# Kernel tuning notes

Hardware: AMD Instinct MI355X
Metric: run time of the kernel (lower is better)

Reference implementation:

```python
import jax, jax.numpy as jnp
import numpy as np
from jax import lax

EPS_BN = 1e-5
EPS_LN = 1e-5
K = 16  # patch size (cubic)
S = 8   # patch stride (cubic)


def _conv3d(x, w, stride):
    # x: [B,C,D,H,W], w: [O,I,kD,kH,kW], padding=1 on all spatial dims (torch padding=1)
    return lax.conv_general_dilated(
        x, w, (stride, stride, stride), [(1, 1), (1, 1), (1, 1)],
        dimension_numbers=('NCDHW', 'OIDHW', 'NCDHW'))


def _bn_relu(x, g, b):
    # train-mode BatchNorm3d: batch statistics over (B, D, H, W) per channel
    mean = jnp.mean(x, axis=(0, 2, 3, 4), keepdims=True)
    var = jnp.var(x, axis=(0, 2, 3, 4), keepdims=True)
    xh = (x - mean) * lax.rsqrt(var + EPS_BN)
    g = g[None, :, None, None, None]
    b = b[None, :, None, None, None]
    return jax.nn.relu(xh * g + b)


def _extract_patches_3d(f0):
    # f0: [B,C,D,H,W] -> patches [B,N,C*K^3] (C-major then kD,kH,kW, matching torch unfold),
    # coords [B,N,3]
    B, C, D, H, W = f0.shape
    Do, Ho, Wo = (D - K) // S + 1, (H - K) // S + 1, (W - K) // S + 1
    di = jnp.arange(Do)[:, None] * S + jnp.arange(K)[None, :]  # [Do,K]
    hi = jnp.arange(Ho)[:, None] * S + jnp.arange(K)[None, :]
    wi = jnp.arange(Wo)[:, None] * S + jnp.arange(K)[None, :]
    p = f0[:, :, di]                 # [B,C,Do,K,H,W]
    p = p[:, :, :, :, hi]            # [B,C,Do,K,Ho,K,W]
    p = p[:, :, :, :, :, :, wi]      # [B,C,Do,K,Ho,K,Wo,K]
    p = p.transpose(0, 2, 4, 6, 1, 3, 5, 7)  # [B,Do,Ho,Wo,C,K,K,K]
    patches = p.reshape(B, Do * Ho * Wo, C * K * K * K)
    half = (K - 1) / 2.0
    z = (jnp.arange(Do) * S + half) / max(D - 1, 1)
    y = (jnp.arange(Ho) * S + half) / max(H - 1, 1)
    xg = (jnp.arange(Wo) * S + half) / max(W - 1, 1)
    zz, yy, xx = jnp.meshgrid(z, y, xg, indexing='ij')
    coords = jnp.stack([zz.reshape(-1), yy.reshape(-1), xx.reshape(-1)], axis=-1)
    coords = jnp.broadcast_to(coords[None], (B,) + coords.shape)
    return patches, coords


def _layer_norm(x, g, b):
    mu = jnp.mean(x, axis=-1, keepdims=True)
    var = jnp.var(x, axis=-1, keepdims=True)
    return (x - mu) * lax.rsqrt(var + EPS_LN) * g + b


def setup_inputs() -> dict:
    key = jax.random.key(0)
    ks = jax.random.split(key, 8)
    C_in, mid, stem, tok_d, aux_d = 1, 16, 32, 128, 32
    pdim = stem * K * K * K  # 131072
    f32 = jnp.float32
    x = jax.random.normal(ks[0], (2, C_in, 128, 128, 128), dtype=f32)
    def kinit(k, shape, fan_in):
        return jax.random.normal(k, shape, dtype=f32) * (1.0 / np.sqrt(fan_in))
    return {
        'x': x,
        'conv1_w': kinit(ks[1], (mid, C_in, 3, 3, 3), C_in * 27),
        'bn1_g': jnp.ones((mid,), f32), 'bn1_b': jnp.zeros((mid,), f32),
        'conv2_w': kinit(ks[2], (mid, mid, 3, 3, 3), mid * 27),
        'bn2_g': jnp.ones((mid,), f32), 'bn2_b': jnp.zeros((mid,), f32),
        'conv3_w': kinit(ks[3], (stem, mid, 3, 3, 3), mid * 27),
        'bn3_g': jnp.ones((stem,), f32), 'bn3_b': jnp.zeros((stem,), f32),
        'tok_w': kinit(ks[4], (tok_d, pdim), pdim), 'tok_b': jnp.zeros((tok_d,), f32),
        'aux_w': kinit(ks[5], (aux_d, pdim), pdim), 'aux_b': jnp.zeros((aux_d,), f32),
        'ln_g': jnp.ones((tok_d,), f32), 'ln_b': jnp.zeros((tok_d,), f32),
    }


def reference(x, conv1_w, bn1_g, bn1_b, conv2_w, bn2_g, bn2_b, conv3_w, bn3_g, bn3_b,
              tok_w, tok_b, aux_w, aux_b, ln_g, ln_b):
    f0 = _bn_relu(_conv3d(x, conv1_w, 1), bn1_g, bn1_b)
    f0 = _bn_relu(_conv3d(f0, conv2_w, 1), bn2_g, bn2_b)
    f0 = _bn_relu(_conv3d(f0, conv3_w, 2), bn3_g, bn3_b)  # [B,32,64,64,64]
    patches, coords = _extract_patches_3d(f0)  # [B,N,131072]
    tokens = jnp.einsum('bnp,tp->bnt', patches, tok_w) + tok_b
    tokens = _layer_norm(tokens, ln_g, ln_b)
    aux = jnp.einsum('bnp,ap->bna', patches, aux_w) + aux_b
    return tokens, aux, coords
```

## Files before the change

kernel.cpp:

```cpp
#include <hip/hip_runtime.h>
#include <hip/hip_bf16.h>


typedef __hip_bfloat16 bf16;
typedef __attribute__((ext_vector_type(8))) short short8;
typedef __attribute__((ext_vector_type(4))) float f32x4;
__device__ __forceinline__ float b2f(bf16 v){ return __bfloat162float(v); }
__device__ __forceinline__ bf16 f2b(float v){ return __float2bfloat16(v); }
__device__ __forceinline__ unsigned short f2bu(float f){
  unsigned u = __float_as_uint(f);
  return (unsigned short)((u + 0x7fff + ((u>>16)&1)) >> 16);
}
__device__ __forceinline__ unsigned cvtpk(float lo, float hi){
  unsigned r;
  asm("v_cvt_pk_bf16_f32 %0, %1, %2" : "=v"(r) : "v"(lo), "v"(hi));
  return r;
}

#define SP12 2097152
#define SP3  262144
#define M_TOT 686
#define TOK_OFF 0
#define AUX_OFF 87808
#define CRD_OFF 109760
#define KSPLIT 64
#define NSLAB 32

__global__ __launch_bounds__(256) void k_packw(const float* __restrict__ w1,
                                               const float* __restrict__ w2,
                                               const float* __restrict__ w3,
                                               unsigned short* __restrict__ wp1,
                                               unsigned short* __restrict__ wp2,
                                               unsigned short* __restrict__ wp3){
  int i = blockIdx.x*256 + threadIdx.x;
  if(i < 512){
    int oc = i>>5, k = i&31;
    float v = (k<27)? w1[oc*27+k] : 0.f;
    wp1[i] = f2bu(v);
  } else if(i < 7680){
    int j = i - 512;
    int oc = j/448, k = j - oc*448;
    int tap = k>>4, ic = k&15;
    float v = (tap<27)? w2[(oc*16+ic)*27+tap] : 0.f;
    wp2[oc*448+k] = f2bu(v);
  } else if(i < 22016){
    int j = i - 7680;
    int oc = j/448, r = j - oc*448;
    int h = r/224, k2 = r - h*224;
    int tap = (k2>>5)*4 + ((k2>>3)&3);
    int ic = h*8 + (k2&7);
    float v = (tap<27)? w3[(oc*16+ic)*27+tap] : 0.f;
    wp3[oc*448 + h*224 + k2] = f2bu(v);
  }
}

#define C1P 88
__global__ __launch_bounds__(256) void k_conv1(const float* __restrict__ x,
                                               const unsigned short* __restrict__ wp1,
                                               unsigned short* __restrict__ y1u,
                                               float* __restrict__ psum){
  __shared__ unsigned short in_l[6*6*C1P];
  int t = threadIdx.x;
  int bx = blockIdx.x;
  int xt = bx&1, yt = (bx>>1)&31, zt = (bx>>6)&31, b = bx>>11;
  int x0 = xt*64, y0 = yt*4, z0 = zt*4;

  for(int i=t; i<648; i+=256){
    int c = i%18; int row = i/18; int yy = row%6; int zz = row/6;
    int gz = z0-1+zz, gy = y0-1+yy;
    bool rowok = ((unsigned)gz<128u) && ((unsigned)gy<128u);
    int gx4 = x0-4+c*4;
    const float* rp = x + (size_t)b*SP12 + (rowok? ((gz<<14)+(gy<<7)) : 0);
    float v0,v1,v2,v3;
    if(rowok && gx4>=0 && gx4<=124){
      float4 v = *(const float4*)(rp + gx4);
      v0=v.x; v1=v.y; v2=v.z; v3=v.w;
    } else {
      float vv[4];
#pragma unroll
      for(int e=0;e<4;e++){
        int gx = gx4+e; bool ok = rowok && ((unsigned)gx<128u);
        float val = rp[ok? gx : 0];
        vv[e] = ok? val : 0.f;
      }
      v0=vv[0]; v1=vv[1]; v2=vv[2]; v3=vv[3];
    }
    uint2 p;
    p.x = cvtpk(v0,v1);
    p.y = cvtpk(v2,v3);
    *(uint2*)&in_l[row*C1P + c*4] = p;
  }
  __syncthreads();

  int lane = t&63, wv = t>>6;
  int m = lane&15, q = lane>>4;
  short8 wfr = *(const short8*)(wp1 + m*32 + q*8);
  int toff[8];
#pragma unroll
  for(int j=0;j<8;j++){
    int tap = q*8+j; if(tap>26) tap=26;
    int dz = tap/9; int rr = tap-dz*9; int dy = rr/3; int dx = rr-dy*3;
    toff[j] = (dz*6+dy)*C1P + dx + 3 + m;
  }
  float s4[4]={0.f,0.f,0.f,0.f}, q4[4]={0.f,0.f,0.f,0.f};
#pragma unroll
  for(int yi=0; yi<4; yi++){
#pragma unroll
    for(int mg=0; mg<4; mg++){
      int base = (wv*6+yi)*C1P + mg*16;
      short8 vf;
#pragma unroll
      for(int j=0;j<8;j++) vf[j] = (short)in_l[base + toff[j]];
      f32x4 acc = (f32x4){0.f,0.f,0.f,0.f};
      acc = __builtin_amdgcn_mfma_f32_16x16x32_bf16(wfr, vf, acc, 0,0,0);
      int gz = z0+wv, gy = y0+yi, gxv = x0 + mg*16 + m;
      size_t vbase = (size_t)((b<<21)|(gz<<14)|(gy<<7)|gxv);
      uint2 pw; pw.x = cvtpk(acc[0],acc[1]); pw.y = cvtpk(acc[2],acc[3]);
      *(uint2*)(y1u + vbase*16 + q*4) = pw;
#pragma unroll
      for(int reg=0; reg<4; reg++){
        float v = acc[reg];
        s4[reg] += v; q4[reg] += v*v;
      }
    }
  }
#pragma unroll
  for(int off=1; off<16; off<<=1){
#pragma unroll
    for(int rg=0;rg<4;rg++){ s4[rg] += __shfl_xor(s4[rg],off); q4[rg] += __shfl_xor(q4[rg],off); }
  }
  __syncthreads();
  float* red = (float*)in_l;
  if(m==0){
#pragma unroll
    for(int rg=0;rg<4;rg++){ red[wv*32 + q*4+rg] = s4[rg]; red[wv*32+16 + q*4+rg] = q4[rg]; }
  }
  __syncthreads();
  if(t<32){
    float tot = red[t]+red[32+t]+red[64+t]+red[96+t];
    atomicAdd(&psum[(blockIdx.x & (NSLAB-1))*64 + t], tot);
  }
}

__global__ void k_finalize(const float* __restrict__ psum, const float* __restrict__ g,
                           const float* __restrict__ bb, float* __restrict__ scsh,
                           int C, float invN){
  int i = threadIdx.x;
  if(i<C){
    float s=0.f, q=0.f;
    for(int sl=0; sl<NSLAB; sl++){ s += psum[sl*64+i]; q += psum[sl*64+C+i]; }
    float mean = s*invN;
    float var  = q*invN - mean*mean;
    float sc = g[i]*rsqrtf(var+1e-5f);
    scsh[i]   = sc;
    scsh[C+i] = bb[i] - mean*sc;
  }
}

__global__ __launch_bounds__(256) void k_conv2(const unsigned short* __restrict__ y1u,
                                               const unsigned short* __restrict__ wp2,
                                               const float* __restrict__ scsh,
                                               unsigned short* __restrict__ y2u,
                                               float* __restrict__ psum2){
  __shared__ unsigned short tile[10*6*18*16];
  __shared__ float s_sc[16], s_sh[16];
  int t = threadIdx.x;
  if(t < 32){ float v = scsh[t]; if(t<16) s_sc[t]=v; else s_sh[t-16]=v; }
  int bx = blockIdx.x;
  int txx = bx&7, tyy=(bx>>3)&31, tzz=(bx>>8)&15, b=bx>>12;
  int x0 = txx*16, y0 = tyy*4, z0 = tzz*8;

  {
    int sxl = t%18, szz = t/18;
    bool sact = t < 180;
    int gx = x0 + sxl - 1, gz = z0 + szz - 1;
    bool szok = sact && ((unsigned)gx<128u) && ((unsigned)gz<128u);
    size_t srow0 = szok ? (size_t)((b<<21)|(gz<<14)|gx) : 0;
    int sw8 = ((sxl>>2)&1)*8;
    int tb = (szz*6*18 + sxl)*16;
    __syncthreads();
    if(sact){
#pragma unroll
      for(int yy=0; yy<6; yy++){
        int gy = y0 + yy - 1;
        bool ok = szok && ((unsigned)gy < 128u);
        uint4 o0; o0.x=0;o0.y=0;o0.z=0;o0.w=0;
        uint4 o1 = o0;
        if(ok){
          const unsigned short* src = y1u + ((srow0 | ((size_t)gy<<7))<<4);
          uint4 u0 = *(const uint4*)src;
          uint4 u1 = *(const uint4*)(src+8);
          unsigned uu[8]; uu[0]=u0.x; uu[1]=u0.y; uu[2]=u0.z; uu[3]=u0.w;
          uu[4]=u1.x; uu[5]=u1.y; uu[6]=u1.z; uu[7]=u1.w;
          unsigned oo[8];
#pragma unroll
          for(int j=0;j<8;j++){
            float lo = fmaxf(__uint_as_float(uu[j]<<16)        *s_sc[2*j]   + s_sh[2*j],   0.f);
            float hi = fmaxf(__uint_as_float(uu[j]&0xffff0000u)*s_sc[2*j+1] + s_sh[2*j+1], 0.f);
            oo[j] = cvtpk(lo, hi);
          }
          o0.x=oo[0]; o0.y=oo[1]; o0.z=oo[2]; o0.w=oo[3];
          o1.x=oo[4]; o1.y=oo[5]; o1.z=oo[6]; o1.w=oo[7];
        }
        unsigned short* dst = &tile[tb + yy*288];
        *(uint4*)(dst + sw8)       = o0;
        *(uint4*)(dst + (8 - sw8)) = o1;
      }
    }
  }
  __syncthreads();

  int lane = t & 63, wid = t>>6;
  int m = lane & 15, q = lane>>4;
  int qh = q&1, qt = q>>1;
  f32x4 acc[8];
#pragma unroll
  for(int r=0;r<8;r++) acc[r] = (f32x4){0.f,0.f,0.f,0.f};
  const char* tbase = (const char*)tile + wid*6912;
  const unsigned short* wrow = wp2 + m*448 + q*8;
#pragma unroll
  for(int kp=0;kp<14;kp++){
    short8 wf = *(const short8*)(wrow + kp*32);
    int tap = kp*2 + qt; if(tap>26) tap=26;
    int dz = tap/9; int rr2 = tap - dz*9; int dy = rr2/3; int dx = rr2 - dy*3;
    int xl = m + dx;
    int abyte = ((dz*6 + dy)*18 + xl)*32 + ((qh ^ ((xl>>2)&1))*16);
    const char* ap = tbase + abyte;
#pragma unroll
    for(int r=0;r<8;r++){
      const short8 vf = *(const short8*)(ap + ((r>>2)*6 + (r&3))*576);
      acc[r] = __builtin_amdgcn_mfma_f32_16x16x32_bf16(wf, vf, acc[r], 0,0,0);
    }
  }

  float s4[4]={0.f,0.f,0.f,0.f}, q4[4]={0.f,0.f,0.f,0.f};
#pragma unroll
  for(int r=0;r<8;r++){
    int gz = z0 + wid*2 + (r>>2), gy = y0 + (r&3);
    size_t vbase = (size_t)((b<<21)|(gz<<14)|(gy<<7)|(x0+m));
    uint2 pw; pw.x = cvtpk(acc[r][0],acc[r][1]); pw.y = cvtpk(acc[r][2],acc[r][3]);
    *(uint2*)(y2u + vbase*16 + q*4) = pw;
#pragma unroll
    for(int reg=0;reg<4;reg++){
      float v = acc[r][reg];
      s4[reg] += v; q4[reg] += v*v;
    }
  }
#pragma unroll
  for(int off=1; off<16; off<<=1){
#pragma unroll
    for(int rg=0;rg<4;rg++){ s4[rg] += __shfl_xor(s4[rg],off); q4[rg] += __shfl_xor(q4[rg],off); }
  }
  __syncthreads();
  float* red = (float*)tile;
  if(m==0){
#pragma unroll
    for(int rg=0;rg<4;rg++){ red[wid*32 + q*4+rg] = s4[rg]; red[wid*32+16 + q*4+rg] = q4[rg]; }
  }
  __syncthreads();
  if(t<32){
    float tot = red[t]+red[32+t]+red[64+t]+red[96+t];
    atomicAdd(&psum2[(blockIdx.x & (NSLAB-1))*64 + t], tot);
  }
}

#define C3PITCH 576
__global__ __launch_bounds__(256) void k_conv3(const unsigned short* __restrict__ y2u,
                                               const unsigned short* __restrict__ wp3,
                                               const float* __restrict__ scsh,
                                               bf16* __restrict__ f0,
                                               float* __restrict__ psum3){
  __shared__ unsigned short tile3[45*288];
  __shared__ float s_sc[16], s_sh[16];
  int t = threadIdx.x;
  if(t < 32){ float v = scsh[t]; if(t<16) s_sc[t]=v; else s_sh[t-16]=v; }
  __syncthreads();
  int bx = blockIdx.x;
  int tx = bx&3, ty=(bx>>2)&15, tz=(bx>>6)&31, b=bx>>11;
  int x0 = tx*16, y0 = ty*4, z0 = tz*2;
  int gx0 = 2*x0-1, gy0 = 2*y0-1, gz0 = 2*z0-1;

  int lane = t & 63, wid = t>>6;
  int m = lane & 15, q = lane>>4;
  f32x4 acc[2][2];
#pragma unroll
  for(int r=0;r<2;r++){ acc[r][0]=(f32x4){0,0,0,0}; acc[r][1]=(f32x4){0,0,0,0}; }
  const unsigned short* wr0 = wp3 + m*448      + q*8;
  const unsigned short* wr1 = wp3 + (16+m)*448 + q*8;

  for(int half=0; half<2; half++){
    for(int i=t;i<1485;i+=256){
      int xl_ = i%33; int r1 = i/33; int yy_ = r1%9; int zz_ = r1/9;
      int gx = gx0+xl_, gy = gy0+yy_, gz = gz0+zz_;
      bool ok = (gx>=0)&&(gy>=0)&&(gz>=0);
      uint4 o; o.x=0;o.y=0;o.z=0;o.w=0;
      if(ok){
        uint4 u = *(const uint4*)(y2u + ((size_t)((b<<21)|(gz<<14)|(gy<<7)|gx))*16 + half*8);
        int c0 = half*8;
        unsigned uu[4]; uu[0]=u.x; uu[1]=u.y; uu[2]=u.z; uu[3]=u.w;
        unsigned oo[4];
#pragma unroll
        for(int j=0;j<4;j++){
          float lo = fmaxf(__uint_as_float(uu[j]<<16)        *s_sc[c0+2*j]   + s_sh[c0+2*j],   0.f);
          float hi = fmaxf(__uint_as_float(uu[j]&0xffff0000u)*s_sc[c0+2*j+1] + s_sh[c0+2*j+1], 0.f);
          oo[j] = cvtpk(lo, hi);
        }
        o.x=oo[0]; o.y=oo[1]; o.z=oo[2]; o.w=oo[3];
      }
      int sb = (xl_<<4) ^ ((xl_&8)<<1) ^ ((xl_&16)<<1);
      *(uint4*)((char*)tile3 + (zz_*9+yy_)*C3PITCH + sb) = o;
    }
    __syncthreads();

    const unsigned short* w0h = wr0 + half*224;
    const unsigned short* w1h = wr1 + half*224;
#pragma unroll
    for(int kp=0;kp<7;kp++){
      short8 bf0 = *(const short8*)(w0h + kp*32);
      short8 bf1 = *(const short8*)(w1h + kp*32);
      int tap = kp*4 + q; if(tap>26) tap=26;
      int dz = tap/9; int rr = tap - dz*9; int dy = rr/3; int dx = rr - dy*3;
      int xl = 2*m + dx;
      int sb = (xl<<4) ^ ((xl&8)<<1) ^ ((xl&16)<<1);
#pragma unroll
      for(int rl=0;rl<2;rl++){
        int row = wid*2 + rl;
        int tz_ = 2*(row>>2) + dz;
        int ty_ = 2*(row&3) + dy;
        const short8 af = *(const short8*)((const char*)tile3 + (tz_*9+ty_)*C3PITCH + sb);
        acc[rl][0] = __builtin_amdgcn_mfma_f32_16x16x32_bf16(af, bf0, acc[rl][0], 0,0,0);
        acc[rl][1] = __builtin_amdgcn_mfma_f32_16x16x32_bf16(af, bf1, acc[rl][1], 0,0,0);
      }
    }
    __syncthreads();
  }

  float s0=0.f,q0=0.f,s1=0.f,q1=0.f;
#pragma unroll
  for(int rl=0;rl<2;rl++){
    int row = wid*2 + rl;
    int oz = z0 + (row>>2), oy = y0 + (row&3);
    size_t sp = (size_t)oz*4096 + oy*64 + x0 + q*4;
#pragma unroll
    for(int oct=0;oct<2;oct++){
      int oc = oct*16 + m;
      bf16* dst = f0 + (size_t)(b*32+oc)*SP3 + sp;
      f32x4 a = acc[rl][oct];
      uint2 pw; pw.x = cvtpk(a[0],a[1]); pw.y = cvtpk(a[2],a[3]);
      *(uint2*)dst = pw;
#pragma unroll
      for(int reg=0;reg<4;reg++){
        float v = a[reg];
        if(oct==0){ s0 += v; q0 += v*v; } else { s1 += v; q1 += v*v; }
      }
    }
  }
  s0 += __shfl_xor(s0,16); s0 += __shfl_xor(s0,32);
  q0 += __shfl_xor(q0,16); q0 += __shfl_xor(q0,32);
  s1 += __shfl_xor(s1,16); s1 += __shfl_xor(s1,32);
  q1 += __shfl_xor(q1,16); q1 += __shfl_xor(q1,32);
  __syncthreads();
  float* red = (float*)tile3;
  if(lane<16){
    red[wid*64+lane]    = s0; red[wid*64+16+lane] = s1;
    red[wid*64+32+lane] = q0; red[wid*64+48+lane] = q1;
  }
  __syncthreads();
  if(t<64){
    float tot = red[t]+red[64+t]+red[128+t]+red[192+t];
    atomicAdd(&psum3[(blockIdx.x & (NSLAB-1))*64 + t], tot);
  }
}

__global__ __launch_bounds__(256) void k_cvtw(const float* __restrict__ tokw,
                                              const float* __restrict__ auxw,
                                              unsigned short* __restrict__ wb){
  int i = blockIdx.x*256 + threadIdx.x;
  int n = i >> 15;
  int g = i & 32767;
  const float* src = (n<128)? tokw + (size_t)n*131072 : auxw + (size_t)(n-128)*131072;
  float4 v = *(const float4*)(src + g*4);
  uint2 pw; pw.x = cvtpk(v.x, v.y); pw.y = cvtpk(v.z, v.w);
  *(uint2*)(wb + (size_t)n*131072 + g*4) = pw;
}

__global__ __launch_bounds__(256) void k_gemm(const bf16* __restrict__ f0,
                                              const unsigned short* __restrict__ wb,
                                              const float* __restrict__ scsh3,
                                              float* __restrict__ out_acc){
  __shared__ unsigned short Al[64*72];
  __shared__ unsigned short Wl[160*72];
  int mblk = blockIdx.x % 11; int ks = blockIdx.x / 11;
  int M0 = mblk*64;
  int c  = ks >> 1; int kh = ks & 1;
  float sc = scsh3[c], sh = scsh3[32+c];
  int t = threadIdx.x;
  int lane = t & 63; int wid = t >> 6;
  int wm = (wid & 1)*32; int wn = (wid >> 1)*80;
  f32x4 acc[2][5];
#pragma unroll
  for(int i=0;i<2;i++)
#pragma unroll
    for(int j=0;j<5;j++) acc[i][j] = (f32x4){0.f,0.f,0.f,0.f};

  int ky_off0 = (t&7)>>1, half0 = t&1;
  int m_a = t>>3;
  int mg1 = M0 + m_a;       if(mg1>685) mg1=685;
  int mg2 = M0 + m_a + 32;  if(mg2>685) mg2=685;
  int b1 = mg1/343, r1 = mg1%343;
  int b2 = mg2/343, r2 = mg2%343;
  int sp1 = ((r1/49)*8)*4096 + (((r1/7)%7)*8)*64 + (r1%7)*8;
  int sp2 = ((r2/49)*8)*4096 + (((r2/7)%7)*8)*64 + (r2%7)*8;
  const bf16* f0c1 = f0 + (size_t)(b1*32+c)*SP3;
  const bf16* f0c2 = f0 + (size_t)(b2*32+c)*SP3;

  for(int bk=0; bk<32; bk++){
    int bk2 = kh*32 + bk;
    int kz = bk2>>2; int kyb = (bk2&3)*4;
    __syncthreads();
#pragma unroll
    for(int p=0;p<5;p++){
      int n = p*32 + (t>>3);
      int koff = (t&7)*8;
      uint4 v = *(const uint4*)(wb + (size_t)n*131072 + c*4096 + bk2*64 + koff);
      *(uint4*)&Wl[n*72 + koff] = v;
    }
    {
      int ky = kyb + ky_off0; int xo = half0*8;
      int ldso = ky_off0*16 + half0*8;
      uint4 u1 = *(const uint4*)(f0c1 + sp1 + kz*4096 + ky*64 + xo);
      uint4 u2 = *(const uint4*)(f0c2 + sp2 + kz*4096 + ky*64 + xo);
      unsigned uu[8]; uu[0]=u1.x; uu[1]=u1.y; uu[2]=u1.z; uu[3]=u1.w;
      uu[4]=u2.x; uu[5]=u2.y; uu[6]=u2.z; uu[7]=u2.w;
      unsigned outw[8];
#pragma unroll
      for(int qq=0;qq<8;qq++){
        float lo = fmaxf(__uint_as_float(uu[qq]<<16)*sc + sh, 0.f);
        float hi = fmaxf(__uint_as_float(uu[qq]&0xffff0000u)*sc + sh, 0.f);
        outw[qq] = cvtpk(lo, hi);
      }
      uint4 w1; w1.x=outw[0]; w1.y=outw[1]; w1.z=outw[2]; w1.w=outw[3];
      uint4 w2; w2.x=outw[4]; w2.y=outw[5]; w2.z=outw[6]; w2.w=outw[7];
      *(uint4*)&Al[m_a*72 + ldso] = w1;
      *(uint4*)&Al[(m_a+32)*72 + ldso] = w2;
    }
    __syncthreads();
#pragma unroll
    for(int kstep=0;kstep<2;kstep++){
      int ko = kstep*32 + (lane>>4)*8;
      short8 af[2], bfr[5];
#pragma unroll
      for(int mt=0;mt<2;mt++)
        af[mt] = *(const short8*)&Al[(wm + mt*16 + (lane&15))*72 + ko];
#pragma unroll
      for(int nt=0;nt<5;nt++)
        bfr[nt] = *(const short8*)&Wl[(wn + nt*16 + (lane&15))*72 + ko];
#pragma unroll
      for(int mt=0;mt<2;mt++)
#pragma unroll
        for(int nt=0;nt<5;nt++)
          acc[mt][nt] = __builtin_amdgcn_mfma_f32_16x16x32_bf16(af[mt], bfr[nt], acc[mt][nt], 0,0,0);
    }
  }
#pragma unroll
  for(int mt=0;mt<2;mt++){
    int mb = M0 + wm + mt*16 + (lane>>4)*4;
#pragma unroll
    for(int nt=0;nt<5;nt++){
      int n = wn + nt*16 + (lane&15);
#pragma unroll
      for(int reg=0;reg<4;reg++){
        int mm = mb + reg;
        if(mm < M_TOT)
          out_acc[((size_t)ks*M_TOT + mm)*160 + n] = acc[mt][nt][reg];
      }
    }
  }
}

__global__ __launch_bounds__(256) void k_final(const float* __restrict__ out_acc,
                                               const float* __restrict__ tok_b,
                                               const float* __restrict__ aux_b,
                                               const float* __restrict__ ln_g,
                                               const float* __restrict__ ln_b,
                                               float* __restrict__ out){
  int m = blockIdx.x;
  int n = threadIdx.x;
  __shared__ float sA[128], sB[128];
  float sum = 0.f;
  if(n < 160){
    for(int ks=0;ks<KSPLIT;ks++) sum += out_acc[((size_t)ks*M_TOT+m)*160 + n];
  }
  float tval = 0.f;
  if(n < 128){
    tval = sum + tok_b[n];
    sA[n] = tval; sB[n] = tval*tval;
  }
  __syncthreads();
  for(int s=64;s>0;s>>=1){
    if(n < s){ sA[n] += sA[n+s]; sB[n] += sB[n+s]; }
    __syncthreads();
  }
  float mean = sA[0]*(1.f/128.f);
  float var  = sB[0]*(1.f/128.f) - mean*mean;
  float rstd = rsqrtf(var + 1e-5f);
  if(n<128){
    out[TOK_OFF + (size_t)m*128 + n] = (tval-mean)*rstd*ln_g[n] + ln_b[n];
  } else if(n<160){
    out[AUX_OFF + (size_t)m*32 + (n-128)] = sum + aux_b[n-128];
  } else if(n<163){
    int j = n-160;
    int pn = m % 343;
    int nz = pn/49, ny=(pn/7)%7, nx=pn%7;
    int g = (j==0)? nz : (j==1)? ny : nx;
    out[CRD_OFF + (size_t)m*3 + j] = (g*8 + 7.5f)*(1.f/63.f);
  }
}

extern "C" void kernel_launch(void* const* d_in, const int* in_sizes, int n_in,
                              void* d_out, int out_size, void* d_ws, size_t ws_size,
                              hipStream_t stream){
  const float* x    = (const float*)d_in[0];
  const float* w1   = (const float*)d_in[1];
  const float* g1   = (const float*)d_in[2];
  const float* b1   = (const float*)d_in[3];
  const float* w2   = (const float*)d_in[4];
  const float* g2   = (const float*)d_in[5];
  const float* b2   = (const float*)d_in[6];
  const float* w3   = (const float*)d_in[7];
  const float* g3   = (const float*)d_in[8];
  const float* b3   = (const float*)d_in[9];
  const float* tokw = (const float*)d_in[10];
  const float* tokb = (const float*)d_in[11];
  const float* auxw = (const float*)d_in[12];
  const float* auxb = (const float*)d_in[13];
  const float* lng  = (const float*)d_in[14];
  const float* lnb  = (const float*)d_in[15];
  float* out = (float*)d_out;

  char* ws = (char*)d_ws;
  unsigned short* y1u = (unsigned short*)ws;
  unsigned short* y2u = (unsigned short*)(ws + 134217728);
  bf16*  f0      = (bf16*)ws;
  float* out_acc = (float*)(ws + 33554432);
  unsigned short* wbf = (unsigned short*)(ws + 67108864);
  float* stats   = (float*)d_out;
  float* psum1 = stats;        float* psum2 = stats+2048; float* psum3 = stats+4096;
  float* scsh1 = stats+6144;   float* scsh2 = stats+6208; float* scsh3 = stats+6272;
  unsigned short* wp2 = (unsigned short*)(stats + 8192);
  unsigned short* wp3 = (unsigned short*)(stats + 12288);
  unsigned short* wp1 = (unsigned short*)(stats + 20480);

  hipMemsetAsync(stats, 0, 6144*sizeof(float), stream);

  k_packw<<<86, 256, 0, stream>>>(w1, w2, w3, wp1, wp2, wp3);
  k_conv1<<<4096, 256, 0, stream>>>(x, wp1, y1u, psum1);
  k_finalize<<<1, 64, 0, stream>>>(psum1, g1, b1, scsh1, 16, 1.f/4194304.f);
  k_conv2<<<8192, 256, 0, stream>>>(y1u, wp2, scsh1, y2u, psum2);
  k_finalize<<<1, 64, 0, stream>>>(psum2, g2, b2, scsh2, 16, 1.f/4194304.f);
  k_conv3<<<4096, 256, 0, stream>>>(y2u, wp3, scsh2, f0, psum3);
  k_finalize<<<1, 64, 0, stream>>>(psum3, g3, b3, scsh3, 32, 1.f/524288.f);
  k_cvtw<<<20480, 256, 0, stream>>>(tokw, auxw, wbf);
  k_gemm<<<704, 256, 0, stream>>>(f0, wbf, scsh3, out_acc);
  k_final<<<686, 256, 0, stream>>>(out_acc, tokb, auxb, lng, lnb, out);
}
```

Baseline: 458.4 us.

## Fuse fp32-to-bf16 weight conversion into GEMM load and remap blocks per XCD

Removes the separate weight conversion kernel and its bf16 weight buffer; the GEMM now loads fp32 token/aux weights and converts them to bf16 while filling shared memory. Blocks are also remapped so that the blocks sharing a K-slice land on the same XCD, improving L2 reuse of the weights. This saves the write and re-read of the converted weights plus one launch, at the cost of doubling weight bytes per GEMM tile load.

```diff
diff --git a/kernel.cpp b/kernel.cpp
--- a/kernel.cpp
+++ b/kernel.cpp
@@ -372,25 +372,16 @@
   }
 }
 
-__global__ __launch_bounds__(256) void k_cvtw(const float* __restrict__ tokw,
+__global__ __launch_bounds__(256) void k_gemm(const bf16* __restrict__ f0,
+                                              const float* __restrict__ tokw,
                                               const float* __restrict__ auxw,
-                                              unsigned short* __restrict__ wb){
-  int i = blockIdx.x*256 + threadIdx.x;
-  int n = i >> 15;
-  int g = i & 32767;
-  const float* src = (n<128)? tokw + (size_t)n*131072 : auxw + (size_t)(n-128)*131072;
-  float4 v = *(const float4*)(src + g*4);
-  uint2 pw; pw.x = cvtpk(v.x, v.y); pw.y = cvtpk(v.z, v.w);
-  *(uint2*)(wb + (size_t)n*131072 + g*4) = pw;
-}
-
-__global__ __launch_bounds__(256) void k_gemm(const bf16* __restrict__ f0,
-                                              const unsigned short* __restrict__ wb,
                                               const float* __restrict__ scsh3,
                                               float* __restrict__ out_acc){
   __shared__ unsigned short Al[64*72];
   __shared__ unsigned short Wl[160*72];
-  int mblk = blockIdx.x % 11; int ks = blockIdx.x / 11;
+  int bid = blockIdx.x;
+  int logical = (bid & 7)*88 + (bid >> 3);
+  int ks = logical/11; int mblk = logical - ks*11;
   int M0 = mblk*64;
   int c  = ks >> 1; int kh = ks & 1;
   float sc = scsh3[c], sh = scsh3[32+c];
@@ -414,16 +405,25 @@
   const bf16* f0c1 = f0 + (size_t)(b1*32+c)*SP3;
   const bf16* f0c2 = f0 + (size_t)(b2*32+c)*SP3;
 
+  int wrow_n = t>>3;
+  int wkoff  = (t&7)*8;
+
   for(int bk=0; bk<32; bk++){
     int bk2 = kh*32 + bk;
     int kz = bk2>>2; int kyb = (bk2&3)*4;
+    size_t kbase = (size_t)c*4096 + bk2*64 + wkoff;
     __syncthreads();
 #pragma unroll
     for(int p=0;p<5;p++){
-      int n = p*32 + (t>>3);
-      int koff = (t&7)*8;
-      uint4 v = *(const uint4*)(wb + (size_t)n*131072 + c*4096 + bk2*64 + koff);
-      *(uint4*)&Wl[n*72 + koff] = v;
+      int n = p*32 + wrow_n;
+      const float* wsrc = (p<4) ? (tokw + (size_t)n*131072)
+                                : (auxw + (size_t)(n-128)*131072);
+      float4 v0 = *(const float4*)(wsrc + kbase);
+      float4 v1 = *(const float4*)(wsrc + kbase + 4);
+      uint4 pw;
+      pw.x = cvtpk(v0.x, v0.y); pw.y = cvtpk(v0.z, v0.w);
+      pw.z = cvtpk(v1.x, v1.y); pw.w = cvtpk(v1.z, v1.w);
+      *(uint4*)&Wl[n*72 + wkoff] = pw;
     }
     {
       int ky = kyb + ky_off0; int xo = half0*8;
@@ -543,7 +543,6 @@
   unsigned short* y2u = (unsigned short*)(ws + 134217728);
   bf16*  f0      = (bf16*)ws;
   float* out_acc = (float*)(ws + 33554432);
-  unsigned short* wbf = (unsigned short*)(ws + 67108864);
   float* stats   = (float*)d_out;
   float* psum1 = stats;        float* psum2 = stats+2048; float* psum3 = stats+4096;
   float* scsh1 = stats+6144;   float* scsh2 = stats+6208; float* scsh3 = stats+6272;
@@ -560,7 +559,6 @@
   k_finalize<<<1, 64, 0, stream>>>(psum2, g2, b2, scsh2, 16, 1.f/4194304.f);
   k_conv3<<<4096, 256, 0, stream>>>(y2u, wp3, scsh2, f0, psum3);
   k_finalize<<<1, 64, 0, stream>>>(psum3, g3, b3, scsh3, 32, 1.f/524288.f);
-  k_cvtw<<<20480, 256, 0, stream>>>(tokw, auxw, wbf);
-  k_gemm<<<704, 256, 0, stream>>>(f0, wbf, scsh3, out_acc);
+  k_gemm<<<704, 256, 0, stream>>>(f0, tokw, auxw, scsh3, out_acc);
   k_final<<<686, 256, 0, stream>>>(out_acc, tokb, auxb, lng, lnb, out);
 }
```

Measured after the change: 463.4 us. Within noise of the previous version (+1.1%).
